# Kernel tuning notes

Hardware: AMD Instinct MI355X
Metric: run time of the kernel (lower is better)

The kernel has to match this reference:

```python
import jax, jax.numpy as jnp
import numpy as np

EMBED_DIM = 1024
Q_DIM = 512
KV_DIM = 512
NUM_HEADS = 16
HEAD_DIM = EMBED_DIM // NUM_HEADS
EPS = 1e-5


def setup_inputs() -> dict:
    key = jax.random.key(0)
    ks = jax.random.split(key, 13)
    B, N1, N2 = 2, 2048, 2048
    s_q = 1.0 / np.sqrt(Q_DIM)
    s_kv = 1.0 / np.sqrt(KV_DIM)
    s_e = 1.0 / np.sqrt(EMBED_DIM)
    return {
        "query": jax.random.normal(ks[0], (B, N1, Q_DIM), jnp.float32),
        "key": jax.random.normal(ks[1], (B, N2, KV_DIM), jnp.float32),
        "value": jax.random.normal(ks[2], (B, N2, KV_DIM), jnp.float32),
        "Wq": jax.random.uniform(ks[3], (Q_DIM, EMBED_DIM), jnp.float32, -s_q, s_q),
        "bq": jax.random.uniform(ks[4], (EMBED_DIM,), jnp.float32, -s_q, s_q),
        "Wk": jax.random.uniform(ks[5], (KV_DIM, EMBED_DIM), jnp.float32, -s_kv, s_kv),
        "bk": jax.random.uniform(ks[6], (EMBED_DIM,), jnp.float32, -s_kv, s_kv),
        "Wv": jax.random.uniform(ks[7], (KV_DIM, EMBED_DIM), jnp.float32, -s_kv, s_kv),
        "bv": jax.random.uniform(ks[8], (EMBED_DIM,), jnp.float32, -s_kv, s_kv),
        "Wo": jax.random.uniform(ks[9], (EMBED_DIM, EMBED_DIM), jnp.float32, -s_e, s_e),
        "bo": jax.random.uniform(ks[10], (EMBED_DIM,), jnp.float32, -s_e, s_e),
        "gamma": jnp.ones((EMBED_DIM,), jnp.float32),
        "beta": jnp.zeros((EMBED_DIM,), jnp.float32),
    }


def reference(query, key, value, Wq, bq, Wk, bk, Wv, bv, Wo, bo, gamma, beta):
    B, N1, _ = query.shape
    _, N2, _ = key.shape
    scale = HEAD_DIM ** (-0.5)
    # projections -> [B, H, N, D]
    Q = (query @ Wq + bq).reshape(B, N1, NUM_HEADS, HEAD_DIM).transpose(0, 2, 1, 3)
    K = (key @ Wk + bk).reshape(B, N2, NUM_HEADS, HEAD_DIM).transpose(0, 2, 1, 3)
    V = (value @ Wv + bv).reshape(B, N2, NUM_HEADS, HEAD_DIM).transpose(0, 2, 1, 3)
    # full score matrix [B, H, N1, N2] (matches original eager attention)
    att = jnp.einsum("bhqd,bhkd->bhqk", Q, K) * scale
    att = jax.nn.softmax(att, axis=-1)
    # dropout is identity in eval mode
    out = jnp.einsum("bhqk,bhkd->bhqd", att, V)  # [B, H, N1, D]
    out = out.transpose(0, 2, 1, 3).reshape(B, N1, EMBED_DIM)
    out = out @ Wo + bo
    # LayerNorm
    mu = out.mean(-1, keepdims=True)
    var = ((out - mu) ** 2).mean(-1, keepdims=True)
    return (out - mu) * jax.lax.rsqrt(var + EPS) * gamma + beta
```

## Files before the change

kernel.cpp:

```cpp
#include <hip/hip_runtime.h>

typedef __bf16 bf16x8 __attribute__((ext_vector_type(8)));
typedef __bf16 bf16x4 __attribute__((ext_vector_type(4)));
typedef float f32x4 __attribute__((ext_vector_type(4)));
typedef unsigned short u16;
typedef unsigned int u32;

__device__ __forceinline__ f32x4 mfma16(bf16x8 a, bf16x8 b, f32x4 c) {
  return __builtin_amdgcn_mfma_f32_16x16x32_bf16(a, b, c, 0, 0, 0);
}

__device__ __forceinline__ void gload_lds16(const void* g, void* l) {
  __builtin_amdgcn_global_load_lds(
      (const __attribute__((address_space(1))) void*)g,
      (__attribute__((address_space(3))) void*)l, 16, 0, 0);
}

__global__ __launch_bounds__(256) void tobf16_3(const float4* __restrict__ a,
                                                const float4* __restrict__ b,
                                                const float4* __restrict__ c,
                                                bf16x4* __restrict__ oa,
                                                bf16x4* __restrict__ ob,
                                                bf16x4* __restrict__ oc, int n4) {
  int i = blockIdx.x * 256 + threadIdx.x;
  if (i >= n4) return;
  const int z = blockIdx.y;
  const float4* in = z == 0 ? a : z == 1 ? b : c;
  bf16x4* out = z == 0 ? oa : z == 1 ? ob : oc;
  float4 v = in[i];
  bf16x4 o;
  o[0] = (__bf16)v.x; o[1] = (__bf16)v.y; o[2] = (__bf16)v.z; o[3] = (__bf16)v.w;
  out[i] = o;
}

__global__ __launch_bounds__(256) void wtrans4(const float* __restrict__ W0,
                                               const float* __restrict__ W1,
                                               const float* __restrict__ W2,
                                               const float* __restrict__ W3,
                                               u16* __restrict__ T0, u16* __restrict__ T1,
                                               u16* __restrict__ T2, u16* __restrict__ T3) {
  const int z = blockIdx.z;
  const int K = (z == 3) ? 1024 : 512;
  const int N = 1024;
  const int k0 = blockIdx.y * 32;
  if (k0 >= K) return;
  const float* W = z == 0 ? W0 : z == 1 ? W1 : z == 2 ? W2 : W3;
  u16* Wt = z == 0 ? T0 : z == 1 ? T1 : z == 2 ? T2 : T3;
  __shared__ float t[32][33];
  const int tx = threadIdx.x, ty = threadIdx.y;
  const int n0 = blockIdx.x * 32;
#pragma unroll
  for (int i = 0; i < 4; ++i)
    t[ty + i * 8][tx] = W[(size_t)(k0 + ty + i * 8) * N + n0 + tx];
  __syncthreads();
#pragma unroll
  for (int i = 0; i < 4; ++i)
    ((__bf16*)Wt)[(size_t)(n0 + ty + i * 8) * K + k0 + tx] = (__bf16)t[tx][ty + i * 8];
}

__global__ __launch_bounds__(256) void vtrans(const u16* __restrict__ Vb,
                                              u16* __restrict__ Vt, int N2) {
  __shared__ __align__(16) u16 t[64][72];
  const int tid = threadIdx.x;
  const int kv0 = blockIdx.x * 64, h = blockIdx.y, b = blockIdx.z;
  const u16* src = Vb + ((size_t)(b * N2 + kv0)) * 1024 + h * 64;
#pragma unroll
  for (int i = 0; i < 2; ++i) {
    int f = i * 256 + tid;
    int r = f >> 3, c = f & 7;
    *(bf16x8*)&t[r][c * 8] = *(const bf16x8*)&src[(size_t)r * 1024 + c * 8];
  }
  __syncthreads();
  u16* dst = Vt + ((size_t)((b * 16 + h) * 64)) * N2 + kv0;
#pragma unroll
  for (int i = 0; i < 2; ++i) {
    int g = i * 256 + tid;
    int d = g >> 3, kc = g & 7;
    union { u16 u[8]; bf16x8 v; } pk;
#pragma unroll
    for (int j = 0; j < 8; ++j) pk.u[j] = t[kc * 8 + j][d];
    *(bf16x8*)&dst[(size_t)d * N2 + kc * 8] = pk.v;
  }
}

template <int OUT_F32, int DBUF>
__device__ __forceinline__ void gemm_body(const u16* __restrict__ A,
                                          const u16* __restrict__ Bt,
                                          const float* __restrict__ bias,
                                          void* __restrict__ Cout,
                                          int M, int N, int K, float scl) {
  constexpr int NB = DBUF ? 2 : 1;
  __shared__ __align__(16) u16 lA[NB][128 * 64];
  __shared__ __align__(16) u16 lB[NB][128 * 64];
  const int tid = threadIdx.x;
  const int w = tid >> 6, l = tid & 63;
  const int li = l & 15, lg = l >> 4;
  const int wm = w & 1, wn = w >> 1;
  const int bm = blockIdx.x * 128, bn = blockIdx.y * 128;

  f32x4 acc[4][4] = {};
  const int nk = K >> 6;

  auto stage = [&](int kt, int bufi) {
    const int k0 = kt << 6;
#pragma unroll
    for (int i = 0; i < 4; ++i) {
      const int c0 = (i * 4 + w) * 64;
      const int f = c0 + l;
      const int r = f >> 3, cs = (f & 7) ^ (r & 7);
      gload_lds16(A + (size_t)(bm + r) * K + k0 + cs * 8, &lA[bufi][c0 * 8]);
      gload_lds16(Bt + (size_t)(bn + r) * K + k0 + cs * 8, &lB[bufi][c0 * 8]);
    }
  };

  int cur = 0;
  if (DBUF) {
    stage(0, 0);
    __syncthreads();
  }

  for (int kt = 0; kt < nk; ++kt) {
    if (DBUF) {
      if (kt + 1 < nk) stage(kt + 1, cur ^ 1);
    } else {
      stage(kt, 0);
      __syncthreads();
    }
    bf16x8 af[4][2], bfr[4][2];
#pragma unroll
    for (int m = 0; m < 4; ++m) {
      const int row = wm * 64 + m * 16 + li;
#pragma unroll
      for (int kk = 0; kk < 2; ++kk) {
        const int kc = (lg + kk * 4) ^ (row & 7);
        af[m][kk] = *(const bf16x8*)&lA[cur][row * 64 + kc * 8];
      }
    }
#pragma unroll
    for (int n = 0; n < 4; ++n) {
      const int row = wn * 64 + n * 16 + li;
#pragma unroll
      for (int kk = 0; kk < 2; ++kk) {
        const int kc = (lg + kk * 4) ^ (row & 7);
        bfr[n][kk] = *(const bf16x8*)&lB[cur][row * 64 + kc * 8];
      }
    }
#pragma unroll
    for (int m = 0; m < 4; ++m)
#pragma unroll
      for (int n = 0; n < 4; ++n) {
        acc[m][n] = mfma16(af[m][0], bfr[n][0], acc[m][n]);
        acc[m][n] = mfma16(af[m][1], bfr[n][1], acc[m][n]);
      }
    __syncthreads();
    if (DBUF) cur ^= 1;
  }

#pragma unroll
  for (int m = 0; m < 4; ++m) {
    const int row0 = bm + wm * 64 + m * 16 + lg * 4;
#pragma unroll
    for (int n = 0; n < 4; ++n) {
      const int col = bn + wn * 64 + n * 16 + li;
      const float bv = bias[col];
#pragma unroll
      for (int r = 0; r < 4; ++r) {
        float v = (acc[m][n][r] + bv) * scl;
        if (OUT_F32)
          ((float*)Cout)[(size_t)(row0 + r) * N + col] = v;
        else
          ((__bf16*)Cout)[(size_t)(row0 + r) * N + col] = (__bf16)v;
      }
    }
  }
}

__global__ __launch_bounds__(256) void gemm_qkv(const u16* __restrict__ xq,
                                                const u16* __restrict__ xk,
                                                const u16* __restrict__ xv,
                                                const u16* __restrict__ wqt,
                                                const u16* __restrict__ wkt,
                                                const u16* __restrict__ wvt,
                                                const float* __restrict__ bq,
                                                const float* __restrict__ bk,
                                                const float* __restrict__ bv,
                                                u16* __restrict__ Qb, u16* __restrict__ Kb,
                                                u16* __restrict__ Vb, float qscale) {
  const int z = blockIdx.z;
  const u16* A = z == 0 ? xq : z == 1 ? xk : xv;
  const u16* Bt = z == 0 ? wqt : z == 1 ? wkt : wvt;
  const float* bias = z == 0 ? bq : z == 1 ? bk : bv;
  u16* C = z == 0 ? Qb : z == 1 ? Kb : Vb;
  gemm_body<0, 0>(A, Bt, bias, C, 4096, 1024, 512, z == 0 ? qscale : 1.0f);
}

__global__ __launch_bounds__(256) void gemm_o(const u16* __restrict__ A,
                                              const u16* __restrict__ Bt,
                                              const float* __restrict__ bias,
                                              u16* __restrict__ C) {
  gemm_body<0, 1>(A, Bt, bias, C, 4096, 1024, 1024, 1.0f);
}

__global__ __launch_bounds__(512) void attn64(const u16* __restrict__ Qb,
                                              const u16* __restrict__ Kb,
                                              const u16* __restrict__ Vt,
                                              u16* __restrict__ Ob,
                                              int N1, int N2) {
  const int tid = threadIdx.x;
  const int w = tid >> 6, l = tid & 63;
  const int li = l & 15, lg = l >> 4;

  const int flat = blockIdx.x + 16 * (blockIdx.y + 16 * blockIdx.z);
  const int xcd = flat & 7, idx = flat >> 3;
  const int qb = idx & 15, pr = idx >> 4;
  const int h = 2 * xcd + (pr & 1);
  const int b = pr >> 1;
  const int q0 = qb * 128;

  __shared__ __align__(16) u16 lK[2][64 * 64];
  __shared__ __align__(16) u16 lV[2][64 * 64];
  __shared__ __align__(16) u32 lP[8][16 * 32];

  const size_t qoff = (size_t)(b * N1 + q0 + w * 16 + li) * 1024 + h * 64;
  const bf16x8 qa0 = *(const bf16x8*)&Qb[qoff + lg * 8];
  const bf16x8 qa1 = *(const bf16x8*)&Qb[qoff + 32 + lg * 8];

  const u16* Kbase = Kb + (size_t)b * N2 * 1024 + h * 64;
  const u16* Vbase = Vt + (size_t)((b * 16 + h) * 64) * N2;

  const int sr = tid >> 3;
  const int sc = (tid & 7) ^ (sr & 7);

  f32x4 o[4] = {};
  float lsum = 0.f;
  u32* lPw = &lP[w][0];
  const int sw = (li & 7) << 2;
  const int ca = lg ^ (li & 7), cb = (lg + 4) ^ (li & 7);

  const int nt = N2 >> 6;
  int cur = 0;
  gload_lds16(Kbase + (size_t)sr * 1024 + sc * 8, &lK[0][w * 512]);
  gload_lds16(Vbase + (size_t)sr * N2 + sc * 8, &lV[0][w * 512]);
  __syncthreads();

  for (int t = 0; t < nt; ++t) {
    if (t + 1 < nt) {
      gload_lds16(Kbase + (size_t)((t + 1) * 64 + sr) * 1024 + sc * 8, &lK[cur ^ 1][w * 512]);
      gload_lds16(Vbase + (size_t)sr * N2 + (t + 1) * 64 + sc * 8, &lV[cur ^ 1][w * 512]);
    }
    const u16* K_ = lK[cur];
    const u16* V_ = lV[cur];

    float s_t = 0.f;
    __builtin_amdgcn_s_setprio(1);
#pragma unroll
    for (int n = 0; n < 4; ++n) {
      const int row = n * 16 + li;
      bf16x8 k0 = *(const bf16x8*)&K_[row * 64 + ca * 8];
      bf16x8 k1 = *(const bf16x8*)&K_[row * 64 + cb * 8];
      f32x4 a = {};
      a = mfma16(k0, qa0, a);
      a = mfma16(k1, qa1, a);
      float p0 = __builtin_amdgcn_exp2f(a[0]);
      float p1 = __builtin_amdgcn_exp2f(a[1]);
      float p2 = __builtin_amdgcn_exp2f(a[2]);
      float p3 = __builtin_amdgcn_exp2f(a[3]);
      s_t += (p0 + p1) + (p2 + p3);
      bf16x4 pk;
      pk[0] = (__bf16)p0; pk[1] = (__bf16)p1; pk[2] = (__bf16)p2; pk[3] = (__bf16)p3;
      *(bf16x4*)&lPw[li * 32 + ((n * 8 + lg * 2) ^ sw)] = pk;
    }
    __builtin_amdgcn_s_setprio(0);
    lsum += s_t;

    __builtin_amdgcn_s_setprio(1);
#pragma unroll
    for (int ks = 0; ks < 2; ++ks) {
      const bf16x8 pf = *(const bf16x8*)&lPw[li * 32 + ((ks * 16 + lg * 4) ^ sw)];
#pragma unroll
      for (int dt = 0; dt < 4; ++dt) {
        const int row = dt * 16 + li;
        const int c = (lg + ks * 4) ^ (li & 7);
        const bf16x8 vf = *(const bf16x8*)&V_[row * 64 + c * 8];
        o[dt] = mfma16(vf, pf, o[dt]);
      }
    }
    __builtin_amdgcn_s_setprio(0);
    __syncthreads();
    cur ^= 1;
  }

  lsum += __shfl_xor(lsum, 16, 64);
  lsum += __shfl_xor(lsum, 32, 64);
  const float inv = 1.f / lsum;

  const size_t orow = (size_t)(b * N1 + q0 + w * 16 + li) * 1024 + h * 64;
#pragma unroll
  for (int dt = 0; dt < 4; ++dt) {
    bf16x4 pk;
#pragma unroll
    for (int r = 0; r < 4; ++r) pk[r] = (__bf16)(o[dt][r] * inv);
    *(bf16x4*)&Ob[orow + dt * 16 + lg * 4] = pk;
  }
}

__global__ __launch_bounds__(256) void lnorm(const u16* __restrict__ X,
                                             const float* __restrict__ gamma,
                                             const float* __restrict__ beta,
                                             float* __restrict__ out) {
  const int row = blockIdx.x;
  const int tid = threadIdx.x;
  const bf16x4 xv = ((const bf16x4*)(X + (size_t)row * 1024))[tid];
  float4 v;
  v.x = (float)xv[0]; v.y = (float)xv[1]; v.z = (float)xv[2]; v.w = (float)xv[3];
  float s = v.x + v.y + v.z + v.w;
  float sq = v.x * v.x + v.y * v.y + v.z * v.z + v.w * v.w;
#pragma unroll
  for (int d = 1; d < 64; d <<= 1) {
    s += __shfl_xor(s, d, 64);
    sq += __shfl_xor(sq, d, 64);
  }
  __shared__ float red[8];
  const int w = tid >> 6, l = tid & 63;
  if (l == 0) { red[w] = s; red[4 + w] = sq; }
  __syncthreads();
  s = red[0] + red[1] + red[2] + red[3];
  sq = red[4] + red[5] + red[6] + red[7];
  const float mu = s * (1.f / 1024.f);
  const float var = sq * (1.f / 1024.f) - mu * mu;
  const float rstd = rsqrtf(var + 1e-5f);
  const float4 g = ((const float4*)gamma)[tid];
  const float4 bb = ((const float4*)beta)[tid];
  float4 o;
  o.x = (v.x - mu) * rstd * g.x + bb.x;
  o.y = (v.y - mu) * rstd * g.y + bb.y;
  o.z = (v.z - mu) * rstd * g.z + bb.z;
  o.w = (v.w - mu) * rstd * g.w + bb.w;
  ((float4*)(out + (size_t)row * 1024))[tid] = o;
}

extern "C" void kernel_launch(void* const* d_in, const int* in_sizes, int n_in,
                              void* d_out, int out_size, void* d_ws, size_t ws_size,
                              hipStream_t stream) {
  const float* query = (const float*)d_in[0];
  const float* key_ = (const float*)d_in[1];
  const float* value = (const float*)d_in[2];
  const float* Wq = (const float*)d_in[3];
  const float* bq = (const float*)d_in[4];
  const float* Wk = (const float*)d_in[5];
  const float* bk = (const float*)d_in[6];
  const float* Wv = (const float*)d_in[7];
  const float* bv = (const float*)d_in[8];
  const float* Wo = (const float*)d_in[9];
  const float* bo = (const float*)d_in[10];
  const float* gamma = (const float*)d_in[11];
  const float* beta = (const float*)d_in[12];

  constexpr int B = 2, N1 = 2048, N2 = 2048, E = 1024, QKD = 512;
  constexpr int M = B * N1;
  const float QSCALE = 0.125f * 1.4426950408889634f;

  char* p = (char*)d_ws;
  auto alloc = [&](size_t bytes) {
    char* r = p;
    p += (bytes + 255) & ~(size_t)255;
    return r;
  };
  u16* xq = (u16*)alloc((size_t)M * QKD * 2);
  u16* xk = (u16*)alloc((size_t)M * QKD * 2);
  u16* xv = (u16*)alloc((size_t)M * QKD * 2);
  u16* wqt = (u16*)alloc((size_t)E * QKD * 2);
  u16* wkt = (u16*)alloc((size_t)E * QKD * 2);
  u16* wvt = (u16*)alloc((size_t)E * QKD * 2);
  u16* wot = (u16*)alloc((size_t)E * E * 2);
  u16* Qb = (u16*)alloc((size_t)M * E * 2);
  u16* Kb = (u16*)alloc((size_t)M * E * 2);
  u16* Vb = (u16*)alloc((size_t)M * E * 2);
  u16* Vt = (u16*)alloc((size_t)M * E * 2);
  u16* ao = (u16*)alloc((size_t)M * E * 2);
  u16* ao2 = (u16*)alloc((size_t)M * E * 2);

  const int n4 = M * QKD / 4;
  tobf16_3<<<dim3((n4 + 255) / 256, 3), 256, 0, stream>>>(
      (const float4*)query, (const float4*)key_, (const float4*)value,
      (bf16x4*)xq, (bf16x4*)xk, (bf16x4*)xv, n4);

  wtrans4<<<dim3(E / 32, 32, 4), dim3(32, 8), 0, stream>>>(
      Wq, Wk, Wv, Wo, wqt, wkt, wvt, wot);

  gemm_qkv<<<dim3(M / 128, E / 128, 3), 256, 0, stream>>>(
      xq, xk, xv, wqt, wkt, wvt, bq, bk, bv, Qb, Kb, Vb, QSCALE);

  vtrans<<<dim3(N2 / 64, 16, B), 256, 0, stream>>>(Vb, Vt, N2);

  attn64<<<dim3(16, 16, B), 512, 0, stream>>>(Qb, Kb, Vt, ao, N1, N2);

  gemm_o<<<dim3(M / 128, E / 128), 256, 0, stream>>>(ao, wot, bo, ao2);

  lnorm<<<M, 256, 0, stream>>>(ao2, gamma, beta, (float*)d_out);
}
```

Baseline: 112.0 us.

## Fuse V transpose into QKV GEMM epilogue and process two query tiles per attention block

The V projection GEMM now writes its output directly in transposed [B,H,D,N2] layout, which removes the separate vtrans kernel and the intermediate Vb buffer. The attention kernel now handles 256 query rows per block (two 128-row sub-tiles per wave), so each loaded K/V tile serves twice as many queries. This halves K/V LDS traffic per query, but the block count drops to 256 and register and LDS use per block grow, which may lower occupancy. The transposed epilogue stores are strided by column, so they coalesce less well.

```diff
diff --git a/kernel.cpp b/kernel.cpp
--- a/kernel.cpp
+++ b/kernel.cpp
@@ -58,32 +58,7 @@
     ((__bf16*)Wt)[(size_t)(n0 + ty + i * 8) * K + k0 + tx] = (__bf16)t[tx][ty + i * 8];
 }
 
-__global__ __launch_bounds__(256) void vtrans(const u16* __restrict__ Vb,
-                                              u16* __restrict__ Vt, int N2) {
-  __shared__ __align__(16) u16 t[64][72];
-  const int tid = threadIdx.x;
-  const int kv0 = blockIdx.x * 64, h = blockIdx.y, b = blockIdx.z;
-  const u16* src = Vb + ((size_t)(b * N2 + kv0)) * 1024 + h * 64;
-#pragma unroll
-  for (int i = 0; i < 2; ++i) {
-    int f = i * 256 + tid;
-    int r = f >> 3, c = f & 7;
-    *(bf16x8*)&t[r][c * 8] = *(const bf16x8*)&src[(size_t)r * 1024 + c * 8];
-  }
-  __syncthreads();
-  u16* dst = Vt + ((size_t)((b * 16 + h) * 64)) * N2 + kv0;
-#pragma unroll
-  for (int i = 0; i < 2; ++i) {
-    int g = i * 256 + tid;
-    int d = g >> 3, kc = g & 7;
-    union { u16 u[8]; bf16x8 v; } pk;
-#pragma unroll
-    for (int j = 0; j < 8; ++j) pk.u[j] = t[kc * 8 + j][d];
-    *(bf16x8*)&dst[(size_t)d * N2 + kc * 8] = pk.v;
-  }
-}
-
-template <int OUT_F32, int DBUF>
+template <int MODE, int DBUF>
 __device__ __forceinline__ void gemm_body(const u16* __restrict__ A,
                                           const u16* __restrict__ Bt,
                                           const float* __restrict__ bias,
@@ -163,13 +138,18 @@
     for (int n = 0; n < 4; ++n) {
       const int col = bn + wn * 64 + n * 16 + li;
       const float bv = bias[col];
-#pragma unroll
-      for (int r = 0; r < 4; ++r) {
-        float v = (acc[m][n][r] + bv) * scl;
-        if (OUT_F32)
-          ((float*)Cout)[(size_t)(row0 + r) * N + col] = v;
-        else
+      if (MODE == 2) {
+        const int bq = row0 >> 11, kv = row0 & 2047;
+        bf16x4 pk;
+#pragma unroll
+        for (int r = 0; r < 4; ++r) pk[r] = (__bf16)((acc[m][n][r] + bv) * scl);
+        *(bf16x4*)&((u16*)Cout)[((size_t)(bq * 1024 + col)) * 2048 + kv] = pk;
+      } else {
+#pragma unroll
+        for (int r = 0; r < 4; ++r) {
+          float v = (acc[m][n][r] + bv) * scl;
           ((__bf16*)Cout)[(size_t)(row0 + r) * N + col] = (__bf16)v;
+        }
       }
     }
   }
@@ -185,13 +165,15 @@
                                                 const float* __restrict__ bk,
                                                 const float* __restrict__ bv,
                                                 u16* __restrict__ Qb, u16* __restrict__ Kb,
-                                                u16* __restrict__ Vb, float qscale) {
+                                                u16* __restrict__ Vt, float qscale) {
   const int z = blockIdx.z;
-  const u16* A = z == 0 ? xq : z == 1 ? xk : xv;
-  const u16* Bt = z == 0 ? wqt : z == 1 ? wkt : wvt;
-  const float* bias = z == 0 ? bq : z == 1 ? bk : bv;
-  u16* C = z == 0 ? Qb : z == 1 ? Kb : Vb;
-  gemm_body<0, 0>(A, Bt, bias, C, 4096, 1024, 512, z == 0 ? qscale : 1.0f);
+  if (z == 0) {
+    gemm_body<0, 0>(xq, wqt, bq, Qb, 4096, 1024, 512, qscale);
+  } else if (z == 1) {
+    gemm_body<0, 0>(xk, wkt, bk, Kb, 4096, 1024, 512, 1.0f);
+  } else {
+    gemm_body<2, 0>(xv, wvt, bv, Vt, 4096, 1024, 512, 1.0f);
+  }
 }
 
 __global__ __launch_bounds__(256) void gemm_o(const u16* __restrict__ A,
@@ -210,20 +192,24 @@
   const int w = tid >> 6, l = tid & 63;
   const int li = l & 15, lg = l >> 4;
 
-  const int flat = blockIdx.x + 16 * (blockIdx.y + 16 * blockIdx.z);
+  const int flat = blockIdx.x + 8 * (blockIdx.y + 16 * blockIdx.z);
   const int xcd = flat & 7, idx = flat >> 3;
-  const int qb = idx & 15, pr = idx >> 4;
+  const int qb = idx & 7, pr = idx >> 3;
   const int h = 2 * xcd + (pr & 1);
   const int b = pr >> 1;
-  const int q0 = qb * 128;
+  const int q0 = qb * 256;
 
   __shared__ __align__(16) u16 lK[2][64 * 64];
   __shared__ __align__(16) u16 lV[2][64 * 64];
-  __shared__ __align__(16) u32 lP[8][16 * 32];
-
-  const size_t qoff = (size_t)(b * N1 + q0 + w * 16 + li) * 1024 + h * 64;
-  const bf16x8 qa0 = *(const bf16x8*)&Qb[qoff + lg * 8];
-  const bf16x8 qa1 = *(const bf16x8*)&Qb[qoff + 32 + lg * 8];
+  __shared__ __align__(16) u32 lP[8][2][16 * 32];
+
+  bf16x8 qa[2][2];
+#pragma unroll
+  for (int s = 0; s < 2; ++s) {
+    const size_t qoff = (size_t)(b * N1 + q0 + s * 128 + w * 16 + li) * 1024 + h * 64;
+    qa[s][0] = *(const bf16x8*)&Qb[qoff + lg * 8];
+    qa[s][1] = *(const bf16x8*)&Qb[qoff + 32 + lg * 8];
+  }
 
   const u16* Kbase = Kb + (size_t)b * N2 * 1024 + h * 64;
   const u16* Vbase = Vt + (size_t)((b * 16 + h) * 64) * N2;
@@ -231,9 +217,10 @@
   const int sr = tid >> 3;
   const int sc = (tid & 7) ^ (sr & 7);
 
-  f32x4 o[4] = {};
-  float lsum = 0.f;
-  u32* lPw = &lP[w][0];
+  f32x4 o[2][4] = {};
+  float lsum0 = 0.f, lsum1 = 0.f;
+  u32* lP0 = &lP[w][0][0];
+  u32* lP1 = &lP[w][1][0];
   const int sw = (li & 7) << 2;
   const int ca = lg ^ (li & 7), cb = (lg + 4) ^ (li & 7);
 
@@ -251,38 +238,51 @@
     const u16* K_ = lK[cur];
     const u16* V_ = lV[cur];
 
-    float s_t = 0.f;
+    float st0 = 0.f, st1 = 0.f;
     __builtin_amdgcn_s_setprio(1);
 #pragma unroll
     for (int n = 0; n < 4; ++n) {
       const int row = n * 16 + li;
       bf16x8 k0 = *(const bf16x8*)&K_[row * 64 + ca * 8];
       bf16x8 k1 = *(const bf16x8*)&K_[row * 64 + cb * 8];
-      f32x4 a = {};
-      a = mfma16(k0, qa0, a);
-      a = mfma16(k1, qa1, a);
+      f32x4 a = {}, a2 = {};
+      a = mfma16(k0, qa[0][0], a);
+      a = mfma16(k1, qa[0][1], a);
+      a2 = mfma16(k0, qa[1][0], a2);
+      a2 = mfma16(k1, qa[1][1], a2);
       float p0 = __builtin_amdgcn_exp2f(a[0]);
       float p1 = __builtin_amdgcn_exp2f(a[1]);
       float p2 = __builtin_amdgcn_exp2f(a[2]);
       float p3 = __builtin_amdgcn_exp2f(a[3]);
-      s_t += (p0 + p1) + (p2 + p3);
+      st0 += (p0 + p1) + (p2 + p3);
       bf16x4 pk;
       pk[0] = (__bf16)p0; pk[1] = (__bf16)p1; pk[2] = (__bf16)p2; pk[3] = (__bf16)p3;
-      *(bf16x4*)&lPw[li * 32 + ((n * 8 + lg * 2) ^ sw)] = pk;
+      *(bf16x4*)&lP0[li * 32 + ((n * 8 + lg * 2) ^ sw)] = pk;
+      float q0p = __builtin_amdgcn_exp2f(a2[0]);
+      float q1p = __builtin_amdgcn_exp2f(a2[1]);
+      float q2p = __builtin_amdgcn_exp2f(a2[2]);
+      float q3p = __builtin_amdgcn_exp2f(a2[3]);
+      st1 += (q0p + q1p) + (q2p + q3p);
+      bf16x4 pk2;
+      pk2[0] = (__bf16)q0p; pk2[1] = (__bf16)q1p; pk2[2] = (__bf16)q2p; pk2[3] = (__bf16)q3p;
+      *(bf16x4*)&lP1[li * 32 + ((n * 8 + lg * 2) ^ sw)] = pk2;
     }
     __builtin_amdgcn_s_setprio(0);
-    lsum += s_t;
+    lsum0 += st0;
+    lsum1 += st1;
 
     __builtin_amdgcn_s_setprio(1);
 #pragma unroll
     for (int ks = 0; ks < 2; ++ks) {
-      const bf16x8 pf = *(const bf16x8*)&lPw[li * 32 + ((ks * 16 + lg * 4) ^ sw)];
+      const bf16x8 pf0 = *(const bf16x8*)&lP0[li * 32 + ((ks * 16 + lg * 4) ^ sw)];
+      const bf16x8 pf1 = *(const bf16x8*)&lP1[li * 32 + ((ks * 16 + lg * 4) ^ sw)];
 #pragma unroll
       for (int dt = 0; dt < 4; ++dt) {
         const int row = dt * 16 + li;
         const int c = (lg + ks * 4) ^ (li & 7);
         const bf16x8 vf = *(const bf16x8*)&V_[row * 64 + c * 8];
-        o[dt] = mfma16(vf, pf, o[dt]);
+        o[0][dt] = mfma16(vf, pf0, o[0][dt]);
+        o[1][dt] = mfma16(vf, pf1, o[1][dt]);
       }
     }
     __builtin_amdgcn_s_setprio(0);
@@ -290,17 +290,24 @@
     cur ^= 1;
   }
 
-  lsum += __shfl_xor(lsum, 16, 64);
-  lsum += __shfl_xor(lsum, 32, 64);
-  const float inv = 1.f / lsum;
-
-  const size_t orow = (size_t)(b * N1 + q0 + w * 16 + li) * 1024 + h * 64;
-#pragma unroll
-  for (int dt = 0; dt < 4; ++dt) {
-    bf16x4 pk;
-#pragma unroll
-    for (int r = 0; r < 4; ++r) pk[r] = (__bf16)(o[dt][r] * inv);
-    *(bf16x4*)&Ob[orow + dt * 16 + lg * 4] = pk;
+  lsum0 += __shfl_xor(lsum0, 16, 64);
+  lsum0 += __shfl_xor(lsum0, 32, 64);
+  lsum1 += __shfl_xor(lsum1, 16, 64);
+  lsum1 += __shfl_xor(lsum1, 32, 64);
+  const float inv0 = 1.f / lsum0;
+  const float inv1 = 1.f / lsum1;
+
+#pragma unroll
+  for (int s = 0; s < 2; ++s) {
+    const float inv = s == 0 ? inv0 : inv1;
+    const size_t orow = (size_t)(b * N1 + q0 + s * 128 + w * 16 + li) * 1024 + h * 64;
+#pragma unroll
+    for (int dt = 0; dt < 4; ++dt) {
+      bf16x4 pk;
+#pragma unroll
+      for (int r = 0; r < 4; ++r) pk[r] = (__bf16)(o[s][dt][r] * inv);
+      *(bf16x4*)&Ob[orow + dt * 16 + lg * 4] = pk;
+    }
   }
 }
 
@@ -375,7 +382,6 @@
   u16* wot = (u16*)alloc((size_t)E * E * 2);
   u16* Qb = (u16*)alloc((size_t)M * E * 2);
   u16* Kb = (u16*)alloc((size_t)M * E * 2);
-  u16* Vb = (u16*)alloc((size_t)M * E * 2);
   u16* Vt = (u16*)alloc((size_t)M * E * 2);
   u16* ao = (u16*)alloc((size_t)M * E * 2);
   u16* ao2 = (u16*)alloc((size_t)M * E * 2);
@@ -389,11 +395,9 @@
       Wq, Wk, Wv, Wo, wqt, wkt, wvt, wot);
 
   gemm_qkv<<<dim3(M / 128, E / 128, 3), 256, 0, stream>>>(
-      xq, xk, xv, wqt, wkt, wvt, bq, bk, bv, Qb, Kb, Vb, QSCALE);
-
-  vtrans<<<dim3(N2 / 64, 16, B), 256, 0, stream>>>(Vb, Vt, N2);
-
-  attn64<<<dim3(16, 16, B), 512, 0, stream>>>(Qb, Kb, Vt, ao, N1, N2);
+      xq, xk, xv, wqt, wkt, wvt, bq, bk, bv, Qb, Kb, Vt, QSCALE);
+
+  attn64<<<dim3(N1 / 256, 16, B), 512, 0, stream>>>(Qb, Kb, Vt, ao, N1, N2);
 
   gemm_o<<<dim3(M / 128, E / 128), 256, 0, stream>>>(ao, wot, bo, ao2);
 
```

After: 113.5 us. About the same (+1.3%).

## Write V transposed from QKV GEMM and split attention KV across two blocks

Applied to the files above, without the earlier changes.

The V projection epilogue now writes its output directly in transposed [b,h,d,kv] layout, which removes the separate vtrans kernel and its round trip through memory. Attention is split-KV: the grid doubles to 1024 blocks and each handles half of the keys. Partial outputs and row sums go to new buffers, and a new combine kernel merges them. This adds occupancy on the GPU's compute units but costs an extra kernel launch and extra partial-result traffic. The softmax uses no running max, so merging the two halves is just a sum of numerators and denominators.

```diff
diff --git a/kernel.cpp b/kernel.cpp
--- a/kernel.cpp
+++ b/kernel.cpp
@@ -58,32 +58,7 @@
     ((__bf16*)Wt)[(size_t)(n0 + ty + i * 8) * K + k0 + tx] = (__bf16)t[tx][ty + i * 8];
 }
 
-__global__ __launch_bounds__(256) void vtrans(const u16* __restrict__ Vb,
-                                              u16* __restrict__ Vt, int N2) {
-  __shared__ __align__(16) u16 t[64][72];
-  const int tid = threadIdx.x;
-  const int kv0 = blockIdx.x * 64, h = blockIdx.y, b = blockIdx.z;
-  const u16* src = Vb + ((size_t)(b * N2 + kv0)) * 1024 + h * 64;
-#pragma unroll
-  for (int i = 0; i < 2; ++i) {
-    int f = i * 256 + tid;
-    int r = f >> 3, c = f & 7;
-    *(bf16x8*)&t[r][c * 8] = *(const bf16x8*)&src[(size_t)r * 1024 + c * 8];
-  }
-  __syncthreads();
-  u16* dst = Vt + ((size_t)((b * 16 + h) * 64)) * N2 + kv0;
-#pragma unroll
-  for (int i = 0; i < 2; ++i) {
-    int g = i * 256 + tid;
-    int d = g >> 3, kc = g & 7;
-    union { u16 u[8]; bf16x8 v; } pk;
-#pragma unroll
-    for (int j = 0; j < 8; ++j) pk.u[j] = t[kc * 8 + j][d];
-    *(bf16x8*)&dst[(size_t)d * N2 + kc * 8] = pk.v;
-  }
-}
-
-template <int OUT_F32, int DBUF>
+template <int MODE, int DBUF>
 __device__ __forceinline__ void gemm_body(const u16* __restrict__ A,
                                           const u16* __restrict__ Bt,
                                           const float* __restrict__ bias,
@@ -163,13 +138,18 @@
     for (int n = 0; n < 4; ++n) {
       const int col = bn + wn * 64 + n * 16 + li;
       const float bv = bias[col];
-#pragma unroll
-      for (int r = 0; r < 4; ++r) {
-        float v = (acc[m][n][r] + bv) * scl;
-        if (OUT_F32)
-          ((float*)Cout)[(size_t)(row0 + r) * N + col] = v;
-        else
+      if (MODE == 2) {
+        const int bq = row0 >> 11, kv = row0 & 2047;
+        bf16x4 pk;
+#pragma unroll
+        for (int r = 0; r < 4; ++r) pk[r] = (__bf16)((acc[m][n][r] + bv) * scl);
+        *(bf16x4*)&((u16*)Cout)[((size_t)(bq * 1024 + col)) * 2048 + kv] = pk;
+      } else {
+#pragma unroll
+        for (int r = 0; r < 4; ++r) {
+          float v = (acc[m][n][r] + bv) * scl;
           ((__bf16*)Cout)[(size_t)(row0 + r) * N + col] = (__bf16)v;
+        }
       }
     }
   }
@@ -185,13 +165,15 @@
                                                 const float* __restrict__ bk,
                                                 const float* __restrict__ bv,
                                                 u16* __restrict__ Qb, u16* __restrict__ Kb,
-                                                u16* __restrict__ Vb, float qscale) {
+                                                u16* __restrict__ Vt, float qscale) {
   const int z = blockIdx.z;
-  const u16* A = z == 0 ? xq : z == 1 ? xk : xv;
-  const u16* Bt = z == 0 ? wqt : z == 1 ? wkt : wvt;
-  const float* bias = z == 0 ? bq : z == 1 ? bk : bv;
-  u16* C = z == 0 ? Qb : z == 1 ? Kb : Vb;
-  gemm_body<0, 0>(A, Bt, bias, C, 4096, 1024, 512, z == 0 ? qscale : 1.0f);
+  if (z == 0) {
+    gemm_body<0, 0>(xq, wqt, bq, Qb, 4096, 1024, 512, qscale);
+  } else if (z == 1) {
+    gemm_body<0, 0>(xk, wkt, bk, Kb, 4096, 1024, 512, 1.0f);
+  } else {
+    gemm_body<2, 0>(xv, wvt, bv, Vt, 4096, 1024, 512, 1.0f);
+  }
 }
 
 __global__ __launch_bounds__(256) void gemm_o(const u16* __restrict__ A,
@@ -204,7 +186,8 @@
 __global__ __launch_bounds__(512) void attn64(const u16* __restrict__ Qb,
                                               const u16* __restrict__ Kb,
                                               const u16* __restrict__ Vt,
-                                              u16* __restrict__ Ob,
+                                              u16* __restrict__ Opart,
+                                              float* __restrict__ Lpart,
                                               int N1, int N2) {
   const int tid = threadIdx.x;
   const int w = tid >> 6, l = tid & 63;
@@ -212,9 +195,10 @@
 
   const int flat = blockIdx.x + 16 * (blockIdx.y + 16 * blockIdx.z);
   const int xcd = flat & 7, idx = flat >> 3;
-  const int qb = idx & 15, pr = idx >> 4;
-  const int h = 2 * xcd + (pr & 1);
-  const int b = pr >> 1;
+  const int qb = idx & 15, rest = idx >> 4;
+  const int h = 2 * xcd + (rest & 1);
+  const int b = (rest >> 1) & 1;
+  const int kvh = rest >> 2;
   const int q0 = qb * 128;
 
   __shared__ __align__(16) u16 lK[2][64 * 64];
@@ -237,14 +221,15 @@
   const int sw = (li & 7) << 2;
   const int ca = lg ^ (li & 7), cb = (lg + 4) ^ (li & 7);
 
-  const int nt = N2 >> 6;
+  const int t0 = kvh * 16;
   int cur = 0;
-  gload_lds16(Kbase + (size_t)sr * 1024 + sc * 8, &lK[0][w * 512]);
-  gload_lds16(Vbase + (size_t)sr * N2 + sc * 8, &lV[0][w * 512]);
+  gload_lds16(Kbase + (size_t)(t0 * 64 + sr) * 1024 + sc * 8, &lK[0][w * 512]);
+  gload_lds16(Vbase + (size_t)sr * N2 + t0 * 64 + sc * 8, &lV[0][w * 512]);
   __syncthreads();
 
-  for (int t = 0; t < nt; ++t) {
-    if (t + 1 < nt) {
+  for (int tt = 0; tt < 16; ++tt) {
+    const int t = t0 + tt;
+    if (tt + 1 < 16) {
       gload_lds16(Kbase + (size_t)((t + 1) * 64 + sr) * 1024 + sc * 8, &lK[cur ^ 1][w * 512]);
       gload_lds16(Vbase + (size_t)sr * N2 + (t + 1) * 64 + sc * 8, &lV[cur ^ 1][w * 512]);
     }
@@ -292,16 +277,35 @@
 
   lsum += __shfl_xor(lsum, 16, 64);
   lsum += __shfl_xor(lsum, 32, 64);
-  const float inv = 1.f / lsum;
-
-  const size_t orow = (size_t)(b * N1 + q0 + w * 16 + li) * 1024 + h * 64;
+
+  const int qrow = b * N1 + q0 + w * 16 + li;
+  u16* Op = Opart + (size_t)kvh * 4096 * 1024;
+  const size_t orow = (size_t)qrow * 1024 + h * 64;
 #pragma unroll
   for (int dt = 0; dt < 4; ++dt) {
     bf16x4 pk;
 #pragma unroll
-    for (int r = 0; r < 4; ++r) pk[r] = (__bf16)(o[dt][r] * inv);
-    *(bf16x4*)&Ob[orow + dt * 16 + lg * 4] = pk;
-  }
+    for (int r = 0; r < 4; ++r) pk[r] = (__bf16)o[dt][r];
+    *(bf16x4*)&Op[orow + dt * 16 + lg * 4] = pk;
+  }
+  if (lg == 0) Lpart[(size_t)kvh * 4096 * 16 + (size_t)qrow * 16 + h] = lsum;
+}
+
+__global__ __launch_bounds__(256) void combine(const u16* __restrict__ Opart,
+                                               const float* __restrict__ Lpart,
+                                               u16* __restrict__ ao) {
+  const int row = blockIdx.x;
+  const int tid = threadIdx.x;
+  const int h = tid >> 4;
+  const float l = Lpart[(size_t)row * 16 + h] + Lpart[4096 * 16 + (size_t)row * 16 + h];
+  const float inv = 1.f / l;
+  const size_t off = (size_t)row * 1024 + tid * 4;
+  const bf16x4 a = *(const bf16x4*)&Opart[off];
+  const bf16x4 b = *(const bf16x4*)&Opart[(size_t)4096 * 1024 + off];
+  bf16x4 o;
+#pragma unroll
+  for (int j = 0; j < 4; ++j) o[j] = (__bf16)(((float)a[j] + (float)b[j]) * inv);
+  *(bf16x4*)&ao[off] = o;
 }
 
 __global__ __launch_bounds__(256) void lnorm(const u16* __restrict__ X,
@@ -375,10 +379,11 @@
   u16* wot = (u16*)alloc((size_t)E * E * 2);
   u16* Qb = (u16*)alloc((size_t)M * E * 2);
   u16* Kb = (u16*)alloc((size_t)M * E * 2);
-  u16* Vb = (u16*)alloc((size_t)M * E * 2);
   u16* Vt = (u16*)alloc((size_t)M * E * 2);
   u16* ao = (u16*)alloc((size_t)M * E * 2);
   u16* ao2 = (u16*)alloc((size_t)M * E * 2);
+  u16* Opart = (u16*)alloc((size_t)2 * M * E * 2);
+  float* Lpart = (float*)alloc((size_t)2 * M * 16 * 4);
 
   const int n4 = M * QKD / 4;
   tobf16_3<<<dim3((n4 + 255) / 256, 3), 256, 0, stream>>>(
@@ -389,11 +394,11 @@
       Wq, Wk, Wv, Wo, wqt, wkt, wvt, wot);
 
   gemm_qkv<<<dim3(M / 128, E / 128, 3), 256, 0, stream>>>(
-      xq, xk, xv, wqt, wkt, wvt, bq, bk, bv, Qb, Kb, Vb, QSCALE);
-
-  vtrans<<<dim3(N2 / 64, 16, B), 256, 0, stream>>>(Vb, Vt, N2);
-
-  attn64<<<dim3(16, 16, B), 512, 0, stream>>>(Qb, Kb, Vt, ao, N1, N2);
+      xq, xk, xv, wqt, wkt, wvt, bq, bk, bv, Qb, Kb, Vt, QSCALE);
+
+  attn64<<<dim3(16, 16, 4), 512, 0, stream>>>(Qb, Kb, Vt, Opart, Lpart, N1, N2);
+
+  combine<<<M, 256, 0, stream>>>(Opart, Lpart, ao);
 
   gemm_o<<<dim3(M / 128, E / 128), 256, 0, stream>>>(ao, wot, bo, ao2);
 
```

Result: slower. 118.0 us (+5.3%).

## Fuse V transpose into QKV GEMM epilogue and keep P in registers

Applied to the files above, without the earlier changes.

The V projection GEMM now writes its output directly in transposed [b, h*d, kv] layout, which removes the separate vtrans kernel and the Vb round trip through memory. In the attention kernel, the softmax probabilities stay in registers and feed 16x16x16 bf16 MFMAs directly. This drops the per-warp LDS P buffer along with its writes and reads. The trade-off is twice as many smaller MFMA instructions with narrower V LDS reads, plus strided 8-byte global stores in the V epilogue.

```diff
diff --git a/kernel.cpp b/kernel.cpp
--- a/kernel.cpp
+++ b/kernel.cpp
@@ -3,11 +3,25 @@
 typedef __bf16 bf16x8 __attribute__((ext_vector_type(8)));
 typedef __bf16 bf16x4 __attribute__((ext_vector_type(4)));
 typedef float f32x4 __attribute__((ext_vector_type(4)));
+typedef short s16x4 __attribute__((ext_vector_type(4)));
 typedef unsigned short u16;
 typedef unsigned int u32;
 
 __device__ __forceinline__ f32x4 mfma16(bf16x8 a, bf16x8 b, f32x4 c) {
   return __builtin_amdgcn_mfma_f32_16x16x32_bf16(a, b, c, 0, 0, 0);
+}
+
+__device__ __forceinline__ f32x4 mfma16k16(bf16x4 a, bf16x4 b, f32x4 c) {
+#if __has_builtin(__builtin_amdgcn_mfma_f32_16x16x16bf16_1k)
+  union { bf16x4 bf; s16x4 s; } ua, ub;
+  ua.bf = a; ub.bf = b;
+  return __builtin_amdgcn_mfma_f32_16x16x16bf16_1k(ua.s, ub.s, c, 0, 0, 0);
+#elif __has_builtin(__builtin_amdgcn_mfma_f32_16x16x16_bf16)
+  return __builtin_amdgcn_mfma_f32_16x16x16_bf16(a, b, c, 0, 0, 0);
+#else
+  asm("v_mfma_f32_16x16x16_bf16 %0, %1, %2, %0" : "+v"(c) : "v"(a), "v"(b));
+  return c;
+#endif
 }
 
 __device__ __forceinline__ void gload_lds16(const void* g, void* l) {
@@ -58,32 +72,7 @@
     ((__bf16*)Wt)[(size_t)(n0 + ty + i * 8) * K + k0 + tx] = (__bf16)t[tx][ty + i * 8];
 }
 
-__global__ __launch_bounds__(256) void vtrans(const u16* __restrict__ Vb,
-                                              u16* __restrict__ Vt, int N2) {
-  __shared__ __align__(16) u16 t[64][72];
-  const int tid = threadIdx.x;
-  const int kv0 = blockIdx.x * 64, h = blockIdx.y, b = blockIdx.z;
-  const u16* src = Vb + ((size_t)(b * N2 + kv0)) * 1024 + h * 64;
-#pragma unroll
-  for (int i = 0; i < 2; ++i) {
-    int f = i * 256 + tid;
-    int r = f >> 3, c = f & 7;
-    *(bf16x8*)&t[r][c * 8] = *(const bf16x8*)&src[(size_t)r * 1024 + c * 8];
-  }
-  __syncthreads();
-  u16* dst = Vt + ((size_t)((b * 16 + h) * 64)) * N2 + kv0;
-#pragma unroll
-  for (int i = 0; i < 2; ++i) {
-    int g = i * 256 + tid;
-    int d = g >> 3, kc = g & 7;
-    union { u16 u[8]; bf16x8 v; } pk;
-#pragma unroll
-    for (int j = 0; j < 8; ++j) pk.u[j] = t[kc * 8 + j][d];
-    *(bf16x8*)&dst[(size_t)d * N2 + kc * 8] = pk.v;
-  }
-}
-
-template <int OUT_F32, int DBUF>
+template <int MODE, int DBUF>
 __device__ __forceinline__ void gemm_body(const u16* __restrict__ A,
                                           const u16* __restrict__ Bt,
                                           const float* __restrict__ bias,
@@ -163,13 +152,18 @@
     for (int n = 0; n < 4; ++n) {
       const int col = bn + wn * 64 + n * 16 + li;
       const float bv = bias[col];
-#pragma unroll
-      for (int r = 0; r < 4; ++r) {
-        float v = (acc[m][n][r] + bv) * scl;
-        if (OUT_F32)
-          ((float*)Cout)[(size_t)(row0 + r) * N + col] = v;
-        else
+      if (MODE == 2) {
+        const int bq = row0 >> 11, kv = row0 & 2047;
+        bf16x4 pk;
+#pragma unroll
+        for (int r = 0; r < 4; ++r) pk[r] = (__bf16)((acc[m][n][r] + bv) * scl);
+        *(bf16x4*)&((u16*)Cout)[((size_t)(bq * 1024 + col)) * 2048 + kv] = pk;
+      } else {
+#pragma unroll
+        for (int r = 0; r < 4; ++r) {
+          float v = (acc[m][n][r] + bv) * scl;
           ((__bf16*)Cout)[(size_t)(row0 + r) * N + col] = (__bf16)v;
+        }
       }
     }
   }
@@ -185,13 +179,15 @@
                                                 const float* __restrict__ bk,
                                                 const float* __restrict__ bv,
                                                 u16* __restrict__ Qb, u16* __restrict__ Kb,
-                                                u16* __restrict__ Vb, float qscale) {
+                                                u16* __restrict__ Vt, float qscale) {
   const int z = blockIdx.z;
-  const u16* A = z == 0 ? xq : z == 1 ? xk : xv;
-  const u16* Bt = z == 0 ? wqt : z == 1 ? wkt : wvt;
-  const float* bias = z == 0 ? bq : z == 1 ? bk : bv;
-  u16* C = z == 0 ? Qb : z == 1 ? Kb : Vb;
-  gemm_body<0, 0>(A, Bt, bias, C, 4096, 1024, 512, z == 0 ? qscale : 1.0f);
+  if (z == 0) {
+    gemm_body<0, 0>(xq, wqt, bq, Qb, 4096, 1024, 512, qscale);
+  } else if (z == 1) {
+    gemm_body<0, 0>(xk, wkt, bk, Kb, 4096, 1024, 512, 1.0f);
+  } else {
+    gemm_body<2, 0>(xv, wvt, bv, Vt, 4096, 1024, 512, 1.0f);
+  }
 }
 
 __global__ __launch_bounds__(256) void gemm_o(const u16* __restrict__ A,
@@ -219,7 +215,6 @@
 
   __shared__ __align__(16) u16 lK[2][64 * 64];
   __shared__ __align__(16) u16 lV[2][64 * 64];
-  __shared__ __align__(16) u32 lP[8][16 * 32];
 
   const size_t qoff = (size_t)(b * N1 + q0 + w * 16 + li) * 1024 + h * 64;
   const bf16x8 qa0 = *(const bf16x8*)&Qb[qoff + lg * 8];
@@ -233,9 +228,10 @@
 
   f32x4 o[4] = {};
   float lsum = 0.f;
-  u32* lPw = &lP[w][0];
-  const int sw = (li & 7) << 2;
-  const int ca = lg ^ (li & 7), cb = (lg + 4) ^ (li & 7);
+  const int li7 = li & 7;
+  const int ca = lg ^ li7, cb = (lg + 4) ^ li7;
+  const int vsub = (lg & 1) * 4;
+  const int lgh = lg >> 1;
 
   const int nt = N2 >> 6;
   int cur = 0;
@@ -252,6 +248,7 @@
     const u16* V_ = lV[cur];
 
     float s_t = 0.f;
+    bf16x4 pk[4];
     __builtin_amdgcn_s_setprio(1);
 #pragma unroll
     for (int n = 0; n < 4; ++n) {
@@ -266,23 +263,21 @@
       float p2 = __builtin_amdgcn_exp2f(a[2]);
       float p3 = __builtin_amdgcn_exp2f(a[3]);
       s_t += (p0 + p1) + (p2 + p3);
-      bf16x4 pk;
-      pk[0] = (__bf16)p0; pk[1] = (__bf16)p1; pk[2] = (__bf16)p2; pk[3] = (__bf16)p3;
-      *(bf16x4*)&lPw[li * 32 + ((n * 8 + lg * 2) ^ sw)] = pk;
+      pk[n][0] = (__bf16)p0; pk[n][1] = (__bf16)p1;
+      pk[n][2] = (__bf16)p2; pk[n][3] = (__bf16)p3;
     }
     __builtin_amdgcn_s_setprio(0);
     lsum += s_t;
 
     __builtin_amdgcn_s_setprio(1);
 #pragma unroll
-    for (int ks = 0; ks < 2; ++ks) {
-      const bf16x8 pf = *(const bf16x8*)&lPw[li * 32 + ((ks * 16 + lg * 4) ^ sw)];
+    for (int n = 0; n < 4; ++n) {
+      const int c0 = ((2 * n + lgh) ^ li7) * 8 + vsub;
 #pragma unroll
       for (int dt = 0; dt < 4; ++dt) {
         const int row = dt * 16 + li;
-        const int c = (lg + ks * 4) ^ (li & 7);
-        const bf16x8 vf = *(const bf16x8*)&V_[row * 64 + c * 8];
-        o[dt] = mfma16(vf, pf, o[dt]);
+        const bf16x4 vf = *(const bf16x4*)&V_[row * 64 + c0];
+        o[dt] = mfma16k16(vf, pk[n], o[dt]);
       }
     }
     __builtin_amdgcn_s_setprio(0);
@@ -297,10 +292,10 @@
   const size_t orow = (size_t)(b * N1 + q0 + w * 16 + li) * 1024 + h * 64;
 #pragma unroll
   for (int dt = 0; dt < 4; ++dt) {
-    bf16x4 pk;
-#pragma unroll
-    for (int r = 0; r < 4; ++r) pk[r] = (__bf16)(o[dt][r] * inv);
-    *(bf16x4*)&Ob[orow + dt * 16 + lg * 4] = pk;
+    bf16x4 pkk;
+#pragma unroll
+    for (int r = 0; r < 4; ++r) pkk[r] = (__bf16)(o[dt][r] * inv);
+    *(bf16x4*)&Ob[orow + dt * 16 + lg * 4] = pkk;
   }
 }
 
@@ -375,7 +370,6 @@
   u16* wot = (u16*)alloc((size_t)E * E * 2);
   u16* Qb = (u16*)alloc((size_t)M * E * 2);
   u16* Kb = (u16*)alloc((size_t)M * E * 2);
-  u16* Vb = (u16*)alloc((size_t)M * E * 2);
   u16* Vt = (u16*)alloc((size_t)M * E * 2);
   u16* ao = (u16*)alloc((size_t)M * E * 2);
   u16* ao2 = (u16*)alloc((size_t)M * E * 2);
@@ -389,9 +383,7 @@
       Wq, Wk, Wv, Wo, wqt, wkt, wvt, wot);
 
   gemm_qkv<<<dim3(M / 128, E / 128, 3), 256, 0, stream>>>(
-      xq, xk, xv, wqt, wkt, wvt, bq, bk, bv, Qb, Kb, Vb, QSCALE);
-
-  vtrans<<<dim3(N2 / 64, 16, B), 256, 0, stream>>>(Vb, Vt, N2);
+      xq, xk, xv, wqt, wkt, wvt, bq, bk, bv, Qb, Kb, Vt, QSCALE);
 
   attn64<<<dim3(16, 16, B), 512, 0, stream>>>(Qb, Kb, Vt, ao, N1, N2);
 
```

Measured after the change: 115.6 us. 3.2% more time.
